# Kernel tuning notes

Measured on AMD Instinct MI355X. Metric: run time of the kernel, lower is better.

## Reference

```python
import jax, jax.numpy as jnp
import numpy as np

B, D_IN, C, P = 8192, 2048, 1000, 256


def setup_inputs() -> dict:
    key = jax.random.key(0)
    ks = jax.random.split(key, 6)
    return {
        "x": jax.random.normal(ks[0], (B, D_IN), dtype=jnp.float32),
        "Wm": jax.random.normal(ks[1], (C, D_IN), dtype=jnp.float32) * (1.0 / np.sqrt(D_IN)),
        "bm": jax.random.normal(ks[2], (C,), dtype=jnp.float32) * 0.01,
        "u": jax.random.normal(ks[3], (P, C), dtype=jnp.float32),
        "v": jax.random.normal(ks[4], (P, C), dtype=jnp.float32),
        "w": jax.random.normal(ks[5], (P, 1), dtype=jnp.float32),
    }


def reference(x, Wm, bm, u, v, w):
    # Backbone: Linear(D_IN -> C) producing per-instance logits (B, C)
    preds = jnp.einsum("bd,cd->bc", x, Wm) + bm
    # Gated attention, fully batched (replaces per-instance Python loop):
    # tanh(u @ pred) * sigmoid(v @ pred)  -> (B, P)
    gated = jnp.tanh(jnp.einsum("bc,pc->bp", preds, u)) * jax.nn.sigmoid(
        jnp.einsum("bc,pc->bp", preds, v)
    )
    scores = (gated @ w).ravel()          # (B,)
    attention = jax.nn.softmax(scores)    # softmax over instances
    total_pred = jnp.sum(preds * attention[:, None])
    return preds, total_pred
```

## Files before the change

kernel.cpp:

```cpp
#include <hip/hip_runtime.h>
#include <hip/hip_fp16.h>

typedef _Float16 half8 __attribute__((ext_vector_type(8)));
typedef float f32x4 __attribute__((ext_vector_type(4)));

#define B_   8192
#define DIN  2048
#define C_   1000
#define CP   1024
#define NP2  512

static const size_t OFF_XH  = 0;
static const size_t OFF_WH  = OFF_XH  + (size_t)B_ * DIN * 2;
static const size_t OFF_UVH = OFF_WH  + (size_t)CP * DIN * 2;
static const size_t OFF_PH  = OFF_UVH + (size_t)NP2 * CP * 2;
static const size_t OFF_SC  = OFF_PH  + (size_t)B_ * CP * 2;
static const size_t OFF_RS  = OFF_SC  + (size_t)B_ * 4;
static const size_t WS_NEED = OFF_RS  + (size_t)B_ * 4;

#define FENCE asm volatile("" ::: "memory")
#define BARRIER do { FENCE; __builtin_amdgcn_s_barrier(); FENCE; } while (0)

__device__ __forceinline__ void gload16(const void* g, void* l) {
  __builtin_amdgcn_global_load_lds(
      (const __attribute__((address_space(1))) void*)g,
      (__attribute__((address_space(3))) void*)l, 16, 0, 0);
}

__global__ __launch_bounds__(256) void prep_kernel(
    const float* __restrict__ x, const float* __restrict__ Wm,
    const float* __restrict__ u, const float* __restrict__ v,
    _Float16* __restrict__ xh, _Float16* __restrict__ wh,
    _Float16* __restrict__ uvh, float* __restrict__ scores,
    float* __restrict__ rowsum)
{
  const long NX  = (long)B_ * DIN / 8;
  const long NW  = (long)CP * DIN / 8;
  const long NUV = (long)NP2 * CP / 8;
  const long NZ  = 2 * (long)B_ / 8;
  const long T   = NX + NW + NUV + NZ;
  for (long idx = (long)blockIdx.x * blockDim.x + threadIdx.x; idx < T;
       idx += (long)gridDim.x * blockDim.x) {
    if (idx < NX) {
      long e = idx * 8;
      float4 p0 = *(const float4*)(x + e);
      float4 p1 = *(const float4*)(x + e + 4);
      half8 h;
      h[0] = (_Float16)p0.x; h[1] = (_Float16)p0.y; h[2] = (_Float16)p0.z; h[3] = (_Float16)p0.w;
      h[4] = (_Float16)p1.x; h[5] = (_Float16)p1.y; h[6] = (_Float16)p1.z; h[7] = (_Float16)p1.w;
      *(half8*)(xh + e) = h;
    } else if (idx < NX + NW) {
      long e = (idx - NX) * 8;
      int row = (int)(e >> 11);
      half8 h;
      if (row < C_) {
        float4 p0 = *(const float4*)(Wm + e);
        float4 p1 = *(const float4*)(Wm + e + 4);
        h[0] = (_Float16)p0.x; h[1] = (_Float16)p0.y; h[2] = (_Float16)p0.z; h[3] = (_Float16)p0.w;
        h[4] = (_Float16)p1.x; h[5] = (_Float16)p1.y; h[6] = (_Float16)p1.z; h[7] = (_Float16)p1.w;
      } else {
        h = (half8)(_Float16)0.f;
      }
      *(half8*)(wh + e) = h;
    } else if (idx < NX + NW + NUV) {
      long e = (idx - NX - NW) * 8;
      int j = (int)(e >> 10);
      int k = (int)(e & 1023);
      const float* src = (j & 1) ? v : u;
      int p = j >> 1;
      half8 h;
      #pragma unroll
      for (int t = 0; t < 8; ++t) {
        int kk = k + t;
        h[t] = (kk < C_) ? (_Float16)src[(size_t)p * C_ + kk] : (_Float16)0.f;
      }
      *(half8*)(uvh + e) = h;
    } else {
      long e = (idx - NX - NW - NUV) * 8;
      float4 z = {0.f, 0.f, 0.f, 0.f};
      if (e < B_) {
        *(float4*)(scores + e) = z; *(float4*)(scores + e + 4) = z;
      } else {
        long r = e - B_;
        *(float4*)(rowsum + r) = z; *(float4*)(rowsum + r + 4) = z;
      }
    }
  }
}

__global__ __launch_bounds__(512) void gemm1_kernel(
    const _Float16* __restrict__ xh, const _Float16* __restrict__ wh,
    const float* __restrict__ bmv, float* __restrict__ preds,
    _Float16* __restrict__ predsh, float* __restrict__ rowsum)
{
  __shared__ _Float16 lds[3 * 24576];
  const int tid  = threadIdx.x;
  const int lane = tid & 63;
  const int w    = tid >> 6;
  const int wm   = w >> 1;
  const int wn   = w & 1;
  const int bm0  = blockIdx.x * 256;
  const int bn0  = blockIdx.y * 128;

  f32x4 acc[4][4] = {};

  const _Float16* srcA[4];
  const _Float16* srcB[2];
  #pragma unroll
  for (int k = 0; k < 4; ++k) {
    int slot = k * 512 + tid;
    int row  = slot >> 3;
    int cb   = (slot & 7) << 4;
    int scb  = cb ^ ((row & 7) << 4);
    srcA[k] = xh + (size_t)(bm0 + row) * DIN + (scb >> 1);
  }
  #pragma unroll
  for (int k = 0; k < 2; ++k) {
    int slot = k * 512 + tid;
    int row  = slot >> 3;
    int cb   = (slot & 7) << 4;
    int scb  = cb ^ ((row & 7) << 4);
    srcB[k] = wh + (size_t)(bn0 + row) * DIN + (scb >> 1);
  }

  int aoff[4][2], boff[4][2];
  #pragma unroll
  for (int m = 0; m < 4; ++m) {
    #pragma unroll
    for (int ks = 0; ks < 2; ++ks) {
      int ra = wm * 64 + m * 16 + (lane & 15);
      int kb = ks * 64 + (lane >> 4) * 16;
      aoff[m][ks] = ra * 128 + (kb ^ ((ra & 7) << 4));
    }
  }
  #pragma unroll
  for (int n = 0; n < 4; ++n) {
    #pragma unroll
    for (int ks = 0; ks < 2; ++ks) {
      int rb = wn * 64 + n * 16 + (lane & 15);
      int kb = ks * 64 + (lane >> 4) * 16;
      boff[n][ks] = 32768 + rb * 128 + (kb ^ ((rb & 7) << 4));
    }
  }

  half8 aLa[2][2], aLb[2][2], aHf[2][2], bLf[2][2], bHf[2][2];

  auto stA = [&](int cs, int k) {
    gload16(srcA[k], (char*)lds + cs * 49152 + k * 8192 + w * 1024);
  };
  auto stB = [&](int cs, int k) {
    gload16(srcB[k], (char*)lds + cs * 49152 + 32768 + k * 8192 + w * 1024);
  };
  auto advance = [&]() {
    #pragma unroll
    for (int k = 0; k < 4; ++k) srcA[k] += 64;
    srcB[0] += 64; srcB[1] += 64;
  };
  auto rdAH = [&](const char* b) {
    #pragma unroll
    for (int m = 0; m < 2; ++m)
      #pragma unroll
      for (int ks = 0; ks < 2; ++ks)
        aHf[m][ks] = *(const half8*)(b + aoff[m + 2][ks]);
  };
  auto rdBH = [&](const char* b) {
    #pragma unroll
    for (int n = 0; n < 2; ++n)
      #pragma unroll
      for (int ks = 0; ks < 2; ++ks)
        bHf[n][ks] = *(const half8*)(b + boff[n + 2][ks]);
  };
  auto rdAL = [&](const char* b, half8 (&d)[2][2]) {
    #pragma unroll
    for (int m = 0; m < 2; ++m)
      #pragma unroll
      for (int ks = 0; ks < 2; ++ks)
        d[m][ks] = *(const half8*)(b + aoff[m][ks]);
  };
  auto rdBL = [&](const char* b) {
    #pragma unroll
    for (int n = 0; n < 2; ++n)
      #pragma unroll
      for (int ks = 0; ks < 2; ++ks)
        bLf[n][ks] = *(const half8*)(b + boff[n][ks]);
  };
  auto mfLL = [&](half8 (&aL)[2][2]) {
    #pragma unroll
    for (int m = 0; m < 2; ++m)
      #pragma unroll
      for (int n = 0; n < 2; ++n)
        #pragma unroll
        for (int ks = 0; ks < 2; ++ks)
          acc[m][n] = __builtin_amdgcn_mfma_f32_16x16x32_f16(aL[m][ks], bLf[n][ks], acc[m][n], 0, 0, 0);
  };
  auto mfHL = [&]() {
    #pragma unroll
    for (int m = 0; m < 2; ++m)
      #pragma unroll
      for (int n = 0; n < 2; ++n)
        #pragma unroll
        for (int ks = 0; ks < 2; ++ks)
          acc[m + 2][n] = __builtin_amdgcn_mfma_f32_16x16x32_f16(aHf[m][ks], bLf[n][ks], acc[m + 2][n], 0, 0, 0);
  };
  auto mfLH = [&](half8 (&aL)[2][2]) {
    #pragma unroll
    for (int m = 0; m < 2; ++m)
      #pragma unroll
      for (int n = 0; n < 2; ++n)
        #pragma unroll
        for (int ks = 0; ks < 2; ++ks)
          acc[m][n + 2] = __builtin_amdgcn_mfma_f32_16x16x32_f16(aL[m][ks], bHf[n][ks], acc[m][n + 2], 0, 0, 0);
  };
  auto mfHH = [&]() {
    #pragma unroll
    for (int m = 0; m < 2; ++m)
      #pragma unroll
      for (int n = 0; n < 2; ++n)
        #pragma unroll
        for (int ks = 0; ks < 2; ++ks)
          acc[m + 2][n + 2] = __builtin_amdgcn_mfma_f32_16x16x32_f16(aHf[m][ks], bHf[n][ks], acc[m + 2][n + 2], 0, 0, 0);
  };

  #pragma unroll
  for (int k = 0; k < 4; ++k) stA(0, k);
  stB(0, 0); stB(0, 1);
  advance();
  #pragma unroll
  for (int k = 0; k < 4; ++k) stA(1, k);
  stB(1, 0); stB(1, 1);
  advance();
  asm volatile("s_waitcnt vmcnt(6)" ::: "memory");
  BARRIER;
  rdAL((const char*)lds, aLa);
  rdBL((const char*)lds);

  int c0 = 0;
  #pragma unroll 1
  for (int t = 0; t < 30; t += 2) {
    const int c1 = (c0 == 2) ? 0 : c0 + 1;
    const int c2 = (c1 == 2) ? 0 : c1 + 1;
    const char* bt  = (const char*)lds + c0 * 49152;
    const char* bn1 = (const char*)lds + c1 * 49152;
    const char* bn2 = (const char*)lds + c2 * 49152;

    rdAH(bt);  stA(c2, 0); stA(c2, 1);
    BARRIER;
    __builtin_amdgcn_s_setprio(1); mfLL(aLa); __builtin_amdgcn_s_setprio(0);

    rdBH(bt);  stA(c2, 2); stA(c2, 3);
    asm volatile("s_waitcnt vmcnt(4)" ::: "memory");
    BARRIER;
    __builtin_amdgcn_s_setprio(1); mfHL(); __builtin_amdgcn_s_setprio(0);

    rdAL(bn1, aLb);  stB(c2, 0);
    BARRIER;
    __builtin_amdgcn_s_setprio(1); mfLH(aLa); __builtin_amdgcn_s_setprio(0);

    rdBL(bn1);  stB(c2, 1); advance();
    BARRIER;
    __builtin_amdgcn_s_setprio(1); mfHH(); __builtin_amdgcn_s_setprio(0);

    rdAH(bn1);  stA(c0, 0); stA(c0, 1);
    BARRIER;
    __builtin_amdgcn_s_setprio(1); mfLL(aLb); __builtin_amdgcn_s_setprio(0);

    rdBH(bn1);  stA(c0, 2); stA(c0, 3);
    asm volatile("s_waitcnt vmcnt(4)" ::: "memory");
    BARRIER;
    __builtin_amdgcn_s_setprio(1); mfHL(); __builtin_amdgcn_s_setprio(0);

    rdAL(bn2, aLa);  stB(c0, 0);
    BARRIER;
    __builtin_amdgcn_s_setprio(1); mfLH(aLb); __builtin_amdgcn_s_setprio(0);

    rdBL(bn2);  stB(c0, 1); advance();
    BARRIER;
    __builtin_amdgcn_s_setprio(1); mfHH(); __builtin_amdgcn_s_setprio(0);

    c0 = c2;
  }

  {
    const char* bt  = (const char*)lds;
    const char* bn1 = (const char*)lds + 49152;
    rdAH(bt);
    BARRIER;
    __builtin_amdgcn_s_setprio(1); mfLL(aLa); __builtin_amdgcn_s_setprio(0);
    rdBH(bt);
    asm volatile("s_waitcnt vmcnt(0)" ::: "memory");
    BARRIER;
    __builtin_amdgcn_s_setprio(1); mfHL(); __builtin_amdgcn_s_setprio(0);
    rdAL(bn1, aLb);
    BARRIER;
    __builtin_amdgcn_s_setprio(1); mfLH(aLa); __builtin_amdgcn_s_setprio(0);
    rdBL(bn1);
    BARRIER;
    __builtin_amdgcn_s_setprio(1); mfHH(); __builtin_amdgcn_s_setprio(0);
    rdAH(bn1); rdBH(bn1);
    mfLL(aLb); mfHL(); mfLH(aLb); mfHH();
  }

  float rp[4][4] = {};
  #pragma unroll
  for (int m = 0; m < 4; ++m) {
    #pragma unroll
    for (int n = 0; n < 4; ++n) {
      f32x4 d = acc[m][n];
      int gc = bn0 + wn * 64 + n * 16 + (lane & 15);
      float bias = (gc < C_) ? bmv[gc] : 0.f;
      #pragma unroll
      for (int j = 0; j < 4; ++j) {
        int gr = bm0 + wm * 64 + m * 16 + (lane >> 4) * 4 + j;
        float val = d[j] + bias;
        predsh[(size_t)gr * CP + gc] = (_Float16)val;
        if (gc < C_) preds[(size_t)gr * C_ + gc] = val;
        rp[m][j] += val;
      }
    }
  }
  #pragma unroll
  for (int m = 0; m < 4; ++m) {
    #pragma unroll
    for (int j = 0; j < 4; ++j) {
      float s = rp[m][j];
      s += __shfl_xor(s, 1); s += __shfl_xor(s, 2);
      s += __shfl_xor(s, 4); s += __shfl_xor(s, 8);
      if ((lane & 15) == 0) {
        int gr = bm0 + wm * 64 + m * 16 + (lane >> 4) * 4 + j;
        atomicAdd(&rowsum[gr], s);
      }
    }
  }
}

__global__ __launch_bounds__(256) void gemm2_kernel(
    const _Float16* __restrict__ predsh, const _Float16* __restrict__ uvh,
    const float* __restrict__ wv, float* __restrict__ scores)
{
  __shared__ _Float16 sA[2][64 * 64];
  __shared__ _Float16 sB[2][128 * 64];
  const int tid  = threadIdx.x;
  const int lane = tid & 63;
  const int w    = tid >> 6;
  const int wm   = w >> 1, wn = w & 1;
  const int bm0  = blockIdx.x * 64;
  const int bn0  = blockIdx.y * 128;

  f32x4 acc[2][4] = {};

  const _Float16* srcA[2]; const _Float16* srcB[4];
  #pragma unroll
  for (int i = 0; i < 2; ++i) {
    int slot = i * 256 + tid;
    int row  = slot >> 3;
    int cb   = (slot & 7) << 4;
    int scb  = cb ^ ((row & 7) << 4);
    srcA[i] = predsh + (size_t)(bm0 + row) * CP + (scb >> 1);
  }
  #pragma unroll
  for (int i = 0; i < 4; ++i) {
    int slot = i * 256 + tid;
    int row  = slot >> 3;
    int cb   = (slot & 7) << 4;
    int scb  = cb ^ ((row & 7) << 4);
    srcB[i] = uvh + (size_t)(bn0 + row) * CP + (scb >> 1);
  }
  int aoff[2][2], boff[4][2];
  #pragma unroll
  for (int ks = 0; ks < 2; ++ks) {
    int kb = ks * 64 + (lane >> 4) * 16;
    #pragma unroll
    for (int mi = 0; mi < 2; ++mi) {
      int ra = wm * 32 + mi * 16 + (lane & 15);
      aoff[mi][ks] = ra * 128 + (kb ^ ((ra & 7) << 4));
    }
    #pragma unroll
    for (int ni = 0; ni < 4; ++ni) {
      int rb = wn * 64 + ni * 16 + (lane & 15);
      boff[ni][ks] = rb * 128 + (kb ^ ((rb & 7) << 4));
    }
  }

  auto stage = [&](int c) {
    #pragma unroll
    for (int i = 0; i < 2; ++i) {
      gload16(srcA[i], &sA[c][(i * 4 + w) * 512]);
      srcA[i] += 64;
    }
    #pragma unroll
    for (int i = 0; i < 4; ++i) {
      gload16(srcB[i], &sB[c][(i * 4 + w) * 512]);
      srcB[i] += 64;
    }
  };

  auto compute = [&](int c) {
    const char* bA = (const char*)&sA[c][0];
    const char* bB = (const char*)&sB[c][0];
    #pragma unroll
    for (int ks = 0; ks < 2; ++ks) {
      half8 a[2], b[4];
      #pragma unroll
      for (int mi = 0; mi < 2; ++mi) a[mi] = *(const half8*)(bA + aoff[mi][ks]);
      #pragma unroll
      for (int ni = 0; ni < 4; ++ni) b[ni] = *(const half8*)(bB + boff[ni][ks]);
      #pragma unroll
      for (int mi = 0; mi < 2; ++mi)
        #pragma unroll
        for (int ni = 0; ni < 4; ++ni)
          acc[mi][ni] = __builtin_amdgcn_mfma_f32_16x16x32_f16(a[mi], b[ni], acc[mi][ni], 0, 0, 0);
    }
  };

  const int NT = CP / 64;
  stage(0);
  #pragma unroll 1
  for (int kt = 0; kt < NT; kt += 2) {
    stage(1);
    asm volatile("s_waitcnt vmcnt(6)" ::: "memory");
    BARRIER;
    compute(0);
    BARRIER;
    if (kt + 2 < NT) {
      stage(0);
      asm volatile("s_waitcnt vmcnt(6)" ::: "memory");
    } else {
      asm volatile("s_waitcnt vmcnt(0)" ::: "memory");
    }
    BARRIER;
    compute(1);
    BARRIER;
  }

  float sp[2][4] = {};
  #pragma unroll
  for (int mi = 0; mi < 2; ++mi) {
    #pragma unroll
    for (int ni = 0; ni < 4; ++ni) {
      f32x4 d = acc[mi][ni];
      int gc = bn0 + wn * 64 + ni * 16 + (lane & 15);
      float wq = wv[gc >> 1];
      bool even = ((gc & 1) == 0);
      #pragma unroll
      for (int j = 0; j < 4; ++j) {
        float t  = d[j];
        float pr = __shfl_xor(t, 1);
        float th = 2.f / (1.f + __expf(-2.f * t)) - 1.f;
        float sg = 1.f / (1.f + __expf(-pr));
        sp[mi][j] += even ? (th * sg * wq) : 0.f;
      }
    }
  }
  #pragma unroll
  for (int mi = 0; mi < 2; ++mi) {
    #pragma unroll
    for (int j = 0; j < 4; ++j) {
      float s = sp[mi][j];
      s += __shfl_xor(s, 1); s += __shfl_xor(s, 2);
      s += __shfl_xor(s, 4); s += __shfl_xor(s, 8);
      if ((lane & 15) == 0) {
        int gr = bm0 + wm * 32 + mi * 16 + (lane >> 4) * 4 + j;
        atomicAdd(&scores[gr], s);
      }
    }
  }
}

__global__ __launch_bounds__(1024) void final_kernel(
    const float* __restrict__ scores, const float* __restrict__ rowsum,
    float* __restrict__ out)
{
  __shared__ float red[16], red2[16];
  const int t = threadIdx.x;
  const int lane = t & 63, wid = t >> 6;
  float s[8];
  float m = -3.4e38f;
  #pragma unroll
  for (int i = 0; i < 8; ++i) { s[i] = scores[t + i * 1024]; m = fmaxf(m, s[i]); }
  #pragma unroll
  for (int off = 1; off < 64; off <<= 1) m = fmaxf(m, __shfl_xor(m, off));
  if (lane == 0) red[wid] = m;
  __syncthreads();
  #pragma unroll
  for (int i = 0; i < 16; ++i) m = fmaxf(m, red[i]);
  __syncthreads();

  float se = 0.f, sr = 0.f;
  #pragma unroll
  for (int i = 0; i < 8; ++i) {
    float e = __expf(s[i] - m);
    se += e;
    sr += e * rowsum[t + i * 1024];
  }
  #pragma unroll
  for (int off = 1; off < 64; off <<= 1) { se += __shfl_xor(se, off); sr += __shfl_xor(sr, off); }
  if (lane == 0) { red[wid] = se; red2[wid] = sr; }
  __syncthreads();
  if (t == 0) {
    float tse = 0.f, tsr = 0.f;
    for (int i = 0; i < 16; ++i) { tse += red[i]; tsr += red2[i]; }
    out[0] = tsr / tse;
  }
}

extern "C" void kernel_launch(void* const* d_in, const int* in_sizes, int n_in,
                              void* d_out, int out_size, void* d_ws, size_t ws_size,
                              hipStream_t stream)
{
  const float* x   = (const float*)d_in[0];
  const float* Wm  = (const float*)d_in[1];
  const float* bmv = (const float*)d_in[2];
  const float* u   = (const float*)d_in[3];
  const float* v   = (const float*)d_in[4];
  const float* wv  = (const float*)d_in[5];
  float* out = (float*)d_out;

  if (ws_size < WS_NEED) return;

  char* ws = (char*)d_ws;
  _Float16* xh     = (_Float16*)(ws + OFF_XH);
  _Float16* wh     = (_Float16*)(ws + OFF_WH);
  _Float16* uvh    = (_Float16*)(ws + OFF_UVH);
  _Float16* predsh = (_Float16*)(ws + OFF_PH);
  float*    scores = (float*)(ws + OFF_SC);
  float*    rowsum = (float*)(ws + OFF_RS);

  prep_kernel<<<2048, 256, 0, stream>>>(x, Wm, u, v, xh, wh, uvh, scores, rowsum);
  gemm1_kernel<<<dim3(32, 8), 512, 0, stream>>>(xh, wh, bmv, out, predsh, rowsum);
  gemm2_kernel<<<dim3(128, 4), 256, 0, stream>>>(predsh, uvh, wv, scores);
  final_kernel<<<1, 1024, 0, stream>>>(scores, rowsum, out + (size_t)B_ * C_);
}
```

Baseline: 90.41 us.

## Fuse fp32-to-fp16 conversion of x into GEMM1 load pipeline

Drops the separate pass that converts x to fp16 in the prep kernel. GEMM1 now loads fp32 x tiles into registers, converts them and writes the swizzled fp16 tiles to LDS, and the software pipeline is restructured around these register loads and their waitcnts. This removes a 64MB read plus 32MB write and re-read of the xh buffer. In exchange, GEMM1 reads x as fp32, which is twice the global bytes that were previously read from the fp16 copy. It also adds VALU conversion work and LDS stores that run inside the main loop alongside the MFMAs.

```diff
diff --git a/kernel.cpp b/kernel.cpp
--- a/kernel.cpp
+++ b/kernel.cpp
@@ -10,8 +10,7 @@
 #define CP   1024
 #define NP2  512
 
-static const size_t OFF_XH  = 0;
-static const size_t OFF_WH  = OFF_XH  + (size_t)B_ * DIN * 2;
+static const size_t OFF_WH  = 0;
 static const size_t OFF_UVH = OFF_WH  + (size_t)CP * DIN * 2;
 static const size_t OFF_PH  = OFF_UVH + (size_t)NP2 * CP * 2;
 static const size_t OFF_SC  = OFF_PH  + (size_t)B_ * CP * 2;
@@ -20,6 +19,8 @@
 
 #define FENCE asm volatile("" ::: "memory")
 #define BARRIER do { FENCE; __builtin_amdgcn_s_barrier(); FENCE; } while (0)
+#define VMCNT(n) asm volatile("s_waitcnt vmcnt(" #n ")" ::: "memory")
+#define LGKM0    asm volatile("s_waitcnt lgkmcnt(0)" ::: "memory")
 
 __device__ __forceinline__ void gload16(const void* g, void* l) {
   __builtin_amdgcn_global_load_lds(
@@ -28,29 +29,19 @@
 }
 
 __global__ __launch_bounds__(256) void prep_kernel(
-    const float* __restrict__ x, const float* __restrict__ Wm,
+    const float* __restrict__ Wm,
     const float* __restrict__ u, const float* __restrict__ v,
-    _Float16* __restrict__ xh, _Float16* __restrict__ wh,
-    _Float16* __restrict__ uvh, float* __restrict__ scores,
-    float* __restrict__ rowsum)
+    _Float16* __restrict__ wh, _Float16* __restrict__ uvh,
+    float* __restrict__ scores, float* __restrict__ rowsum)
 {
-  const long NX  = (long)B_ * DIN / 8;
   const long NW  = (long)CP * DIN / 8;
   const long NUV = (long)NP2 * CP / 8;
   const long NZ  = 2 * (long)B_ / 8;
-  const long T   = NX + NW + NUV + NZ;
+  const long T   = NW + NUV + NZ;
   for (long idx = (long)blockIdx.x * blockDim.x + threadIdx.x; idx < T;
        idx += (long)gridDim.x * blockDim.x) {
-    if (idx < NX) {
+    if (idx < NW) {
       long e = idx * 8;
-      float4 p0 = *(const float4*)(x + e);
-      float4 p1 = *(const float4*)(x + e + 4);
-      half8 h;
-      h[0] = (_Float16)p0.x; h[1] = (_Float16)p0.y; h[2] = (_Float16)p0.z; h[3] = (_Float16)p0.w;
-      h[4] = (_Float16)p1.x; h[5] = (_Float16)p1.y; h[6] = (_Float16)p1.z; h[7] = (_Float16)p1.w;
-      *(half8*)(xh + e) = h;
-    } else if (idx < NX + NW) {
-      long e = (idx - NX) * 8;
       int row = (int)(e >> 11);
       half8 h;
       if (row < C_) {
@@ -62,8 +53,8 @@
         h = (half8)(_Float16)0.f;
       }
       *(half8*)(wh + e) = h;
-    } else if (idx < NX + NW + NUV) {
-      long e = (idx - NX - NW) * 8;
+    } else if (idx < NW + NUV) {
+      long e = (idx - NW) * 8;
       int j = (int)(e >> 10);
       int k = (int)(e & 1023);
       const float* src = (j & 1) ? v : u;
@@ -76,7 +67,7 @@
       }
       *(half8*)(uvh + e) = h;
     } else {
-      long e = (idx - NX - NW - NUV) * 8;
+      long e = (idx - NW - NUV) * 8;
       float4 z = {0.f, 0.f, 0.f, 0.f};
       if (e < B_) {
         *(float4*)(scores + e) = z; *(float4*)(scores + e + 4) = z;
@@ -89,11 +80,12 @@
 }
 
 __global__ __launch_bounds__(512) void gemm1_kernel(
-    const _Float16* __restrict__ xh, const _Float16* __restrict__ wh,
+    const float* __restrict__ x, const _Float16* __restrict__ wh,
     const float* __restrict__ bmv, float* __restrict__ preds,
     _Float16* __restrict__ predsh, float* __restrict__ rowsum)
 {
-  __shared__ _Float16 lds[3 * 24576];
+  __shared__ _Float16 lds[3 * 16384 + 3 * 8192];
+  char* const LB = (char*)lds;
   const int tid  = threadIdx.x;
   const int lane = tid & 63;
   const int w    = tid >> 6;
@@ -104,16 +96,17 @@
 
   f32x4 acc[4][4] = {};
 
-  const _Float16* srcA[4];
+  const float* srcAx[4];
+  int dstAoff[4];
+  #pragma unroll
+  for (int j = 0; j < 4; ++j) {
+    int slot = j * 512 + tid;
+    int row  = slot >> 3;
+    int col8 = slot & 7;
+    srcAx[j]   = x + (size_t)(bm0 + row) * DIN + col8 * 8;
+    dstAoff[j] = row * 128 + ((col8 << 4) ^ ((row & 7) << 4));
+  }
   const _Float16* srcB[2];
-  #pragma unroll
-  for (int k = 0; k < 4; ++k) {
-    int slot = k * 512 + tid;
-    int row  = slot >> 3;
-    int cb   = (slot & 7) << 4;
-    int scb  = cb ^ ((row & 7) << 4);
-    srcA[k] = xh + (size_t)(bm0 + row) * DIN + (scb >> 1);
-  }
   #pragma unroll
   for (int k = 0; k < 2; ++k) {
     int slot = k * 512 + tid;
@@ -139,21 +132,38 @@
     for (int ks = 0; ks < 2; ++ks) {
       int rb = wn * 64 + n * 16 + (lane & 15);
       int kb = ks * 64 + (lane >> 4) * 16;
-      boff[n][ks] = 32768 + rb * 128 + (kb ^ ((rb & 7) << 4));
+      boff[n][ks] = rb * 128 + (kb ^ ((rb & 7) << 4));
     }
   }
 
   half8 aLa[2][2], aLb[2][2], aHf[2][2], bLf[2][2], bHf[2][2];
-
-  auto stA = [&](int cs, int k) {
-    gload16(srcA[k], (char*)lds + cs * 49152 + k * 8192 + w * 1024);
-  };
-  auto stB = [&](int cs, int k) {
-    gload16(srcB[k], (char*)lds + cs * 49152 + 32768 + k * 8192 + w * 1024);
-  };
-  auto advance = [&]() {
-    #pragma unroll
-    for (int k = 0; k < 4; ++k) srcA[k] += 64;
+  float4 af[4][2];
+
+  auto issueA01 = [&]() {
+    af[0][0] = *(const float4*)srcAx[0]; af[0][1] = *(const float4*)(srcAx[0] + 4);
+    af[1][0] = *(const float4*)srcAx[1]; af[1][1] = *(const float4*)(srcAx[1] + 4);
+  };
+  auto issueA23 = [&]() {
+    af[2][0] = *(const float4*)srcAx[2]; af[2][1] = *(const float4*)(srcAx[2] + 4);
+    af[3][0] = *(const float4*)srcAx[3]; af[3][1] = *(const float4*)(srcAx[3] + 4);
+    #pragma unroll
+    for (int j = 0; j < 4; ++j) srcAx[j] += 64;
+  };
+  auto cvtWriteA = [&](int cbuf) {
+    char* base = LB + cbuf * 32768;
+    #pragma unroll
+    for (int j = 0; j < 4; ++j) {
+      half8 h;
+      h[0] = (_Float16)af[j][0].x; h[1] = (_Float16)af[j][0].y;
+      h[2] = (_Float16)af[j][0].z; h[3] = (_Float16)af[j][0].w;
+      h[4] = (_Float16)af[j][1].x; h[5] = (_Float16)af[j][1].y;
+      h[6] = (_Float16)af[j][1].z; h[7] = (_Float16)af[j][1].w;
+      *(half8*)(base + dstAoff[j]) = h;
+    }
+  };
+  auto stB = [&](int cbuf) {
+    gload16(srcB[0], LB + 98304 + cbuf * 16384 + w * 1024);
+    gload16(srcB[1], LB + 98304 + cbuf * 16384 + 8192 + w * 1024);
     srcB[0] += 64; srcB[1] += 64;
   };
   auto rdAH = [&](const char* b) {
@@ -221,82 +231,101 @@
           acc[m + 2][n + 2] = __builtin_amdgcn_mfma_f32_16x16x32_f16(aHf[m][ks], bHf[n][ks], acc[m + 2][n + 2], 0, 0, 0);
   };
 
-  #pragma unroll
-  for (int k = 0; k < 4; ++k) stA(0, k);
-  stB(0, 0); stB(0, 1);
-  advance();
-  #pragma unroll
-  for (int k = 0; k < 4; ++k) stA(1, k);
-  stB(1, 0); stB(1, 1);
-  advance();
-  asm volatile("s_waitcnt vmcnt(6)" ::: "memory");
+  #define PRIO1 __builtin_amdgcn_s_setprio(1)
+  #define PRIO0 __builtin_amdgcn_s_setprio(0)
+
+  issueA01(); issueA23();
+  stB(0);
+  VMCNT(2);
+  cvtWriteA(0);
+  issueA01(); issueA23();
+  stB(1);
+  VMCNT(10);
+  LGKM0;
   BARRIER;
-  rdAL((const char*)lds, aLa);
-  rdBL((const char*)lds);
+  rdAL(LB, aLa);
+  rdBL(LB + 98304);
 
   int c0 = 0;
   #pragma unroll 1
   for (int t = 0; t < 30; t += 2) {
     const int c1 = (c0 == 2) ? 0 : c0 + 1;
     const int c2 = (c1 == 2) ? 0 : c1 + 1;
-    const char* bt  = (const char*)lds + c0 * 49152;
-    const char* bn1 = (const char*)lds + c1 * 49152;
-    const char* bn2 = (const char*)lds + c2 * 49152;
-
-    rdAH(bt);  stA(c2, 0); stA(c2, 1);
-    BARRIER;
-    __builtin_amdgcn_s_setprio(1); mfLL(aLa); __builtin_amdgcn_s_setprio(0);
-
-    rdBH(bt);  stA(c2, 2); stA(c2, 3);
-    asm volatile("s_waitcnt vmcnt(4)" ::: "memory");
-    BARRIER;
-    __builtin_amdgcn_s_setprio(1); mfHL(); __builtin_amdgcn_s_setprio(0);
-
-    rdAL(bn1, aLb);  stB(c2, 0);
-    BARRIER;
-    __builtin_amdgcn_s_setprio(1); mfLH(aLa); __builtin_amdgcn_s_setprio(0);
-
-    rdBL(bn1);  stB(c2, 1); advance();
-    BARRIER;
-    __builtin_amdgcn_s_setprio(1); mfHH(); __builtin_amdgcn_s_setprio(0);
-
-    rdAH(bn1);  stA(c0, 0); stA(c0, 1);
-    BARRIER;
-    __builtin_amdgcn_s_setprio(1); mfLL(aLb); __builtin_amdgcn_s_setprio(0);
-
-    rdBH(bn1);  stA(c0, 2); stA(c0, 3);
-    asm volatile("s_waitcnt vmcnt(4)" ::: "memory");
-    BARRIER;
-    __builtin_amdgcn_s_setprio(1); mfHL(); __builtin_amdgcn_s_setprio(0);
-
-    rdAL(bn2, aLa);  stB(c0, 0);
-    BARRIER;
-    __builtin_amdgcn_s_setprio(1); mfLH(aLb); __builtin_amdgcn_s_setprio(0);
-
-    rdBL(bn2);  stB(c0, 1); advance();
-    BARRIER;
-    __builtin_amdgcn_s_setprio(1); mfHH(); __builtin_amdgcn_s_setprio(0);
+    const char* pA0 = LB + c0 * 32768;
+    const char* pA1 = LB + c1 * 32768;
+    const char* pA2 = LB + c2 * 32768;
+    const char* pB0 = LB + 98304 + c0 * 16384;
+    const char* pB1 = LB + 98304 + c1 * 16384;
+    const char* pB2 = LB + 98304 + c2 * 16384;
+
+    VMCNT(2);
+    cvtWriteA(c1);
+    rdAH(pA0);
+    issueA01();
+    LGKM0; BARRIER;
+    PRIO1; mfLL(aLa); PRIO0;
+
+    rdBH(pB0);
+    issueA23();
+    BARRIER;
+    PRIO1; mfHL(); PRIO0;
+
+    rdAL(pA1, aLb);
+    stB(c2);
+    BARRIER;
+    PRIO1; mfLH(aLa); PRIO0;
+
+    VMCNT(10);
+    BARRIER;
+    rdBL(pB1);
+    PRIO1; mfHH(); PRIO0;
+
+    VMCNT(2);
+    cvtWriteA(c2);
+    rdAH(pA1);
+    issueA01();
+    LGKM0; BARRIER;
+    PRIO1; mfLL(aLb); PRIO0;
+
+    rdBH(pB1);
+    issueA23();
+    BARRIER;
+    PRIO1; mfHL(); PRIO0;
+
+    rdAL(pA2, aLa);
+    stB(c0);
+    BARRIER;
+    PRIO1; mfLH(aLb); PRIO0;
+
+    VMCNT(10);
+    BARRIER;
+    rdBL(pB2);
+    PRIO1; mfHH(); PRIO0;
 
     c0 = c2;
   }
 
   {
-    const char* bt  = (const char*)lds;
-    const char* bn1 = (const char*)lds + 49152;
-    rdAH(bt);
-    BARRIER;
-    __builtin_amdgcn_s_setprio(1); mfLL(aLa); __builtin_amdgcn_s_setprio(0);
-    rdBH(bt);
-    asm volatile("s_waitcnt vmcnt(0)" ::: "memory");
-    BARRIER;
-    __builtin_amdgcn_s_setprio(1); mfHL(); __builtin_amdgcn_s_setprio(0);
-    rdAL(bn1, aLb);
-    BARRIER;
-    __builtin_amdgcn_s_setprio(1); mfLH(aLa); __builtin_amdgcn_s_setprio(0);
-    rdBL(bn1);
-    BARRIER;
-    __builtin_amdgcn_s_setprio(1); mfHH(); __builtin_amdgcn_s_setprio(0);
-    rdAH(bn1); rdBH(bn1);
+    const char* pA0 = LB;
+    const char* pA1 = LB + 32768;
+    const char* pB0 = LB + 98304;
+    const char* pB1 = LB + 98304 + 16384;
+    VMCNT(2);
+    cvtWriteA(1);
+    rdAH(pA0);
+    LGKM0; BARRIER;
+    PRIO1; mfLL(aLa); PRIO0;
+    rdBH(pB0);
+    BARRIER;
+    PRIO1; mfHL(); PRIO0;
+    rdAL(pA1, aLb);
+    BARRIER;
+    PRIO1; mfLH(aLa); PRIO0;
+    VMCNT(0);
+    BARRIER;
+    rdBL(pB1);
+    PRIO1; mfHH(); PRIO0;
+    rdAH(pA1); rdBH(pB1);
     mfLL(aLb); mfHL(); mfLH(aLb); mfHH();
   }
 
@@ -331,6 +360,8 @@
       }
     }
   }
+  #undef PRIO1
+  #undef PRIO0
 }
 
 __global__ __launch_bounds__(256) void gemm2_kernel(
@@ -518,15 +549,14 @@
   if (ws_size < WS_NEED) return;
 
   char* ws = (char*)d_ws;
-  _Float16* xh     = (_Float16*)(ws + OFF_XH);
   _Float16* wh     = (_Float16*)(ws + OFF_WH);
   _Float16* uvh    = (_Float16*)(ws + OFF_UVH);
   _Float16* predsh = (_Float16*)(ws + OFF_PH);
   float*    scores = (float*)(ws + OFF_SC);
   float*    rowsum = (float*)(ws + OFF_RS);
 
-  prep_kernel<<<2048, 256, 0, stream>>>(x, Wm, u, v, xh, wh, uvh, scores, rowsum);
-  gemm1_kernel<<<dim3(32, 8), 512, 0, stream>>>(xh, wh, bmv, out, predsh, rowsum);
+  prep_kernel<<<1288, 256, 0, stream>>>(Wm, u, v, wh, uvh, scores, rowsum);
+  gemm1_kernel<<<dim3(32, 8), 512, 0, stream>>>(x, wh, bmv, out, predsh, rowsum);
   gemm2_kernel<<<dim3(128, 4), 256, 0, stream>>>(predsh, uvh, wv, scores);
   final_kernel<<<1, 1024, 0, stream>>>(scores, rowsum, out + (size_t)B_ * C_);
 }
```

After: 91.46 us. Within noise of the previous version (+1.2%).

## Enlarge per-wave tiles and triple-buffer both GEMM kernels with finer-grained pipeline

Applied to the files above, without the earlier changes.

gemm1 drops from 512 to 256 threads per block while keeping the 256x128 block tile, so each wave now computes a 128x64 tile with 32 accumulators. The main loop is also rewritten to one K-step per iteration with interleaved quarter-tile MFMA groups. gemm2 moves from a double-buffered 64x128 tile to a triple-buffered 128x128 tile using the same four-phase staggered LDS read / global-to-LDS load schedule, which halves its grid. The aim is to raise MFMA work per LDS read and improve overlap of loads with compute, at the cost of higher register pressure (launch_bounds 256,1) and fewer waves per CU to hide latency.

```diff
diff --git a/kernel.cpp b/kernel.cpp
--- a/kernel.cpp
+++ b/kernel.cpp
@@ -20,6 +20,9 @@
 
 #define FENCE asm volatile("" ::: "memory")
 #define BARRIER do { FENCE; __builtin_amdgcn_s_barrier(); FENCE; } while (0)
+#define VMCNT(n) asm volatile("s_waitcnt vmcnt(" #n ")" ::: "memory")
+#define PRIO1 __builtin_amdgcn_s_setprio(1)
+#define PRIO0 __builtin_amdgcn_s_setprio(0)
 
 __device__ __forceinline__ void gload16(const void* g, void* l) {
   __builtin_amdgcn_global_load_lds(
@@ -88,12 +91,13 @@
   }
 }
 
-__global__ __launch_bounds__(512) void gemm1_kernel(
+__global__ __launch_bounds__(256, 1) void gemm1_kernel(
     const _Float16* __restrict__ xh, const _Float16* __restrict__ wh,
     const float* __restrict__ bmv, float* __restrict__ preds,
     _Float16* __restrict__ predsh, float* __restrict__ rowsum)
 {
-  __shared__ _Float16 lds[3 * 24576];
+  __shared__ _Float16 lds[(3 * 32768 + 3 * 16384) / 2];
+  char* const LB = (char*)lds;
   const int tid  = threadIdx.x;
   const int lane = tid & 63;
   const int w    = tid >> 6;
@@ -102,207 +106,176 @@
   const int bm0  = blockIdx.x * 256;
   const int bn0  = blockIdx.y * 128;
 
-  f32x4 acc[4][4] = {};
-
-  const _Float16* srcA[4];
-  const _Float16* srcB[2];
-  #pragma unroll
-  for (int k = 0; k < 4; ++k) {
-    int slot = k * 512 + tid;
-    int row  = slot >> 3;
-    int cb   = (slot & 7) << 4;
-    int scb  = cb ^ ((row & 7) << 4);
-    srcA[k] = xh + (size_t)(bm0 + row) * DIN + (scb >> 1);
-  }
-  #pragma unroll
-  for (int k = 0; k < 2; ++k) {
-    int slot = k * 512 + tid;
-    int row  = slot >> 3;
-    int cb   = (slot & 7) << 4;
-    int scb  = cb ^ ((row & 7) << 4);
-    srcB[k] = wh + (size_t)(bn0 + row) * DIN + (scb >> 1);
-  }
-
-  int aoff[4][2], boff[4][2];
-  #pragma unroll
-  for (int m = 0; m < 4; ++m) {
+  f32x4 acc[8][4] = {};
+
+  const int trow = tid >> 3;
+  const int swzc = (((tid & 7) << 4) ^ ((trow & 7) << 4)) >> 1;
+  const _Float16* pA = xh + (size_t)(bm0 + trow) * DIN + swzc;
+  const _Float16* pB = wh + (size_t)(bn0 + trow) * DIN + swzc;
+
+  int aoff[8][2], boff[4][2];
+  #pragma unroll
+  for (int m = 0; m < 8; ++m)
     #pragma unroll
     for (int ks = 0; ks < 2; ++ks) {
-      int ra = wm * 64 + m * 16 + (lane & 15);
+      int ra = wm * 128 + m * 16 + (lane & 15);
       int kb = ks * 64 + (lane >> 4) * 16;
       aoff[m][ks] = ra * 128 + (kb ^ ((ra & 7) << 4));
     }
-  }
-  #pragma unroll
-  for (int n = 0; n < 4; ++n) {
+  #pragma unroll
+  for (int n = 0; n < 4; ++n)
     #pragma unroll
     for (int ks = 0; ks < 2; ++ks) {
       int rb = wn * 64 + n * 16 + (lane & 15);
       int kb = ks * 64 + (lane >> 4) * 16;
-      boff[n][ks] = 32768 + rb * 128 + (kb ^ ((rb & 7) << 4));
-    }
-  }
-
-  half8 aLa[2][2], aLb[2][2], aHf[2][2], bLf[2][2], bHf[2][2];
-
-  auto stA = [&](int cs, int k) {
-    gload16(srcA[k], (char*)lds + cs * 49152 + k * 8192 + w * 1024);
-  };
-  auto stB = [&](int cs, int k) {
-    gload16(srcB[k], (char*)lds + cs * 49152 + 32768 + k * 8192 + w * 1024);
-  };
-  auto advance = [&]() {
-    #pragma unroll
-    for (int k = 0; k < 4; ++k) srcA[k] += 64;
-    srcB[0] += 64; srcB[1] += 64;
-  };
-  auto rdAH = [&](const char* b) {
-    #pragma unroll
-    for (int m = 0; m < 2; ++m)
-      #pragma unroll
-      for (int ks = 0; ks < 2; ++ks)
-        aHf[m][ks] = *(const half8*)(b + aoff[m + 2][ks]);
-  };
-  auto rdBH = [&](const char* b) {
+      boff[n][ks] = rb * 128 + (kb ^ ((rb & 7) << 4));
+    }
+
+  half8 A[8][2], Bf[4][2];
+
+  auto stA = [&](int c, int k) {
+    gload16(pA + (size_t)k * 32 * DIN, LB + c * 32768 + k * 4096 + w * 1024);
+  };
+  auto stB = [&](int c, int k) {
+    gload16(pB + (size_t)k * 32 * DIN, LB + 98304 + c * 16384 + k * 4096 + w * 1024);
+  };
+  auto advance = [&]() { pA += 64; pB += 64; };
+
+  auto rdAL = [&](int c) {
+    const char* b = LB + c * 32768;
+    #pragma unroll
+    for (int m = 0; m < 4; ++m)
+      #pragma unroll
+      for (int ks = 0; ks < 2; ++ks)
+        A[m][ks] = *(const half8*)(b + aoff[m][ks]);
+  };
+  auto rdAH = [&](int c) {
+    const char* b = LB + c * 32768;
+    #pragma unroll
+    for (int m = 4; m < 8; ++m)
+      #pragma unroll
+      for (int ks = 0; ks < 2; ++ks)
+        A[m][ks] = *(const half8*)(b + aoff[m][ks]);
+  };
+  auto rdBL = [&](int c) {
+    const char* b = LB + 98304 + c * 16384;
     #pragma unroll
     for (int n = 0; n < 2; ++n)
       #pragma unroll
       for (int ks = 0; ks < 2; ++ks)
-        bHf[n][ks] = *(const half8*)(b + boff[n + 2][ks]);
-  };
-  auto rdAL = [&](const char* b, half8 (&d)[2][2]) {
-    #pragma unroll
-    for (int m = 0; m < 2; ++m)
-      #pragma unroll
-      for (int ks = 0; ks < 2; ++ks)
-        d[m][ks] = *(const half8*)(b + aoff[m][ks]);
-  };
-  auto rdBL = [&](const char* b) {
-    #pragma unroll
-    for (int n = 0; n < 2; ++n)
-      #pragma unroll
-      for (int ks = 0; ks < 2; ++ks)
-        bLf[n][ks] = *(const half8*)(b + boff[n][ks]);
-  };
-  auto mfLL = [&](half8 (&aL)[2][2]) {
-    #pragma unroll
-    for (int m = 0; m < 2; ++m)
+        Bf[n][ks] = *(const half8*)(b + boff[n][ks]);
+  };
+  auto rdBH = [&](int c) {
+    const char* b = LB + 98304 + c * 16384;
+    #pragma unroll
+    for (int n = 2; n < 4; ++n)
+      #pragma unroll
+      for (int ks = 0; ks < 2; ++ks)
+        Bf[n][ks] = *(const half8*)(b + boff[n][ks]);
+  };
+  auto mfALBL = [&]() {
+    #pragma unroll
+    for (int m = 0; m < 4; ++m)
       #pragma unroll
       for (int n = 0; n < 2; ++n)
         #pragma unroll
         for (int ks = 0; ks < 2; ++ks)
-          acc[m][n] = __builtin_amdgcn_mfma_f32_16x16x32_f16(aL[m][ks], bLf[n][ks], acc[m][n], 0, 0, 0);
-  };
-  auto mfHL = [&]() {
-    #pragma unroll
-    for (int m = 0; m < 2; ++m)
+          acc[m][n] = __builtin_amdgcn_mfma_f32_16x16x32_f16(A[m][ks], Bf[n][ks], acc[m][n], 0, 0, 0);
+  };
+  auto mfAHBL = [&]() {
+    #pragma unroll
+    for (int m = 4; m < 8; ++m)
       #pragma unroll
       for (int n = 0; n < 2; ++n)
         #pragma unroll
         for (int ks = 0; ks < 2; ++ks)
-          acc[m + 2][n] = __builtin_amdgcn_mfma_f32_16x16x32_f16(aHf[m][ks], bLf[n][ks], acc[m + 2][n], 0, 0, 0);
-  };
-  auto mfLH = [&](half8 (&aL)[2][2]) {
-    #pragma unroll
-    for (int m = 0; m < 2; ++m)
-      #pragma unroll
-      for (int n = 0; n < 2; ++n)
+          acc[m][n] = __builtin_amdgcn_mfma_f32_16x16x32_f16(A[m][ks], Bf[n][ks], acc[m][n], 0, 0, 0);
+  };
+  auto mfALBH = [&]() {
+    #pragma unroll
+    for (int m = 0; m < 4; ++m)
+      #pragma unroll
+      for (int n = 2; n < 4; ++n)
         #pragma unroll
         for (int ks = 0; ks < 2; ++ks)
-          acc[m][n + 2] = __builtin_amdgcn_mfma_f32_16x16x32_f16(aL[m][ks], bHf[n][ks], acc[m][n + 2], 0, 0, 0);
-  };
-  auto mfHH = [&]() {
-    #pragma unroll
-    for (int m = 0; m < 2; ++m)
-      #pragma unroll
-      for (int n = 0; n < 2; ++n)
+          acc[m][n] = __builtin_amdgcn_mfma_f32_16x16x32_f16(A[m][ks], Bf[n][ks], acc[m][n], 0, 0, 0);
+  };
+  auto mfAHBH = [&]() {
+    #pragma unroll
+    for (int m = 4; m < 8; ++m)
+      #pragma unroll
+      for (int n = 2; n < 4; ++n)
         #pragma unroll
         for (int ks = 0; ks < 2; ++ks)
-          acc[m + 2][n + 2] = __builtin_amdgcn_mfma_f32_16x16x32_f16(aHf[m][ks], bHf[n][ks], acc[m + 2][n + 2], 0, 0, 0);
-  };
-
-  #pragma unroll
-  for (int k = 0; k < 4; ++k) stA(0, k);
-  stB(0, 0); stB(0, 1);
+          acc[m][n] = __builtin_amdgcn_mfma_f32_16x16x32_f16(A[m][ks], Bf[n][ks], acc[m][n], 0, 0, 0);
+  };
+
+  #pragma unroll
+  for (int k = 0; k < 8; ++k) stA(0, k);
+  #pragma unroll
+  for (int k = 0; k < 4; ++k) stB(0, k);
   advance();
   #pragma unroll
-  for (int k = 0; k < 4; ++k) stA(1, k);
-  stB(1, 0); stB(1, 1);
+  for (int k = 0; k < 8; ++k) stA(1, k);
+  #pragma unroll
+  for (int k = 0; k < 4; ++k) stB(1, k);
   advance();
-  asm volatile("s_waitcnt vmcnt(6)" ::: "memory");
+  VMCNT(12);
   BARRIER;
-  rdAL((const char*)lds, aLa);
-  rdBL((const char*)lds);
+  rdAL(0); rdBL(0);
 
   int c0 = 0;
   #pragma unroll 1
-  for (int t = 0; t < 30; t += 2) {
+  for (int t = 0; t < 30; ++t) {
     const int c1 = (c0 == 2) ? 0 : c0 + 1;
     const int c2 = (c1 == 2) ? 0 : c1 + 1;
-    const char* bt  = (const char*)lds + c0 * 49152;
-    const char* bn1 = (const char*)lds + c1 * 49152;
-    const char* bn2 = (const char*)lds + c2 * 49152;
-
-    rdAH(bt);  stA(c2, 0); stA(c2, 1);
-    BARRIER;
-    __builtin_amdgcn_s_setprio(1); mfLL(aLa); __builtin_amdgcn_s_setprio(0);
-
-    rdBH(bt);  stA(c2, 2); stA(c2, 3);
-    asm volatile("s_waitcnt vmcnt(4)" ::: "memory");
-    BARRIER;
-    __builtin_amdgcn_s_setprio(1); mfHL(); __builtin_amdgcn_s_setprio(0);
-
-    rdAL(bn1, aLb);  stB(c2, 0);
-    BARRIER;
-    __builtin_amdgcn_s_setprio(1); mfLH(aLa); __builtin_amdgcn_s_setprio(0);
-
-    rdBL(bn1);  stB(c2, 1); advance();
-    BARRIER;
-    __builtin_amdgcn_s_setprio(1); mfHH(); __builtin_amdgcn_s_setprio(0);
-
-    rdAH(bn1);  stA(c0, 0); stA(c0, 1);
-    BARRIER;
-    __builtin_amdgcn_s_setprio(1); mfLL(aLb); __builtin_amdgcn_s_setprio(0);
-
-    rdBH(bn1);  stA(c0, 2); stA(c0, 3);
-    asm volatile("s_waitcnt vmcnt(4)" ::: "memory");
-    BARRIER;
-    __builtin_amdgcn_s_setprio(1); mfHL(); __builtin_amdgcn_s_setprio(0);
-
-    rdAL(bn2, aLa);  stB(c0, 0);
-    BARRIER;
-    __builtin_amdgcn_s_setprio(1); mfLH(aLb); __builtin_amdgcn_s_setprio(0);
-
-    rdBL(bn2);  stB(c0, 1); advance();
-    BARRIER;
-    __builtin_amdgcn_s_setprio(1); mfHH(); __builtin_amdgcn_s_setprio(0);
-
-    c0 = c2;
+
+    rdAH(c0);
+    stA(c2, 0); stA(c2, 1); stA(c2, 2);
+    BARRIER;
+    PRIO1; mfALBL(); PRIO0;
+
+    rdBH(c0);
+    stA(c2, 3); stA(c2, 4); stA(c2, 5);
+    VMCNT(6);
+    BARRIER;
+    PRIO1; mfAHBL(); PRIO0;
+
+    rdBL(c1);
+    stA(c2, 6); stA(c2, 7); stB(c2, 0);
+    BARRIER;
+    PRIO1; mfALBH(); PRIO0;
+
+    rdAL(c1);
+    stB(c2, 1); stB(c2, 2); stB(c2, 3);
+    advance();
+    BARRIER;
+    PRIO1; mfAHBH(); PRIO0;
+
+    c0 = c1;
   }
 
   {
-    const char* bt  = (const char*)lds;
-    const char* bn1 = (const char*)lds + 49152;
-    rdAH(bt);
-    BARRIER;
-    __builtin_amdgcn_s_setprio(1); mfLL(aLa); __builtin_amdgcn_s_setprio(0);
-    rdBH(bt);
-    asm volatile("s_waitcnt vmcnt(0)" ::: "memory");
-    BARRIER;
-    __builtin_amdgcn_s_setprio(1); mfHL(); __builtin_amdgcn_s_setprio(0);
-    rdAL(bn1, aLb);
-    BARRIER;
-    __builtin_amdgcn_s_setprio(1); mfLH(aLa); __builtin_amdgcn_s_setprio(0);
-    rdBL(bn1);
-    BARRIER;
-    __builtin_amdgcn_s_setprio(1); mfHH(); __builtin_amdgcn_s_setprio(0);
-    rdAH(bn1); rdBH(bn1);
-    mfLL(aLb); mfHL(); mfLH(aLb); mfHH();
-  }
-
-  float rp[4][4] = {};
-  #pragma unroll
-  for (int m = 0; m < 4; ++m) {
+    rdAH(0);
+    BARRIER;
+    PRIO1; mfALBL(); PRIO0;
+    rdBH(0);
+    VMCNT(0);
+    BARRIER;
+    PRIO1; mfAHBL(); PRIO0;
+    rdBL(1);
+    BARRIER;
+    PRIO1; mfALBH(); PRIO0;
+    rdAL(1);
+    BARRIER;
+    PRIO1; mfAHBH(); PRIO0;
+    rdAH(1); rdBH(1);
+    mfALBL(); mfAHBL(); mfALBH(); mfAHBH();
+  }
+
+  float rp[8][4] = {};
+  #pragma unroll
+  for (int m = 0; m < 8; ++m) {
     #pragma unroll
     for (int n = 0; n < 4; ++n) {
       f32x4 d = acc[m][n];
@@ -310,7 +283,7 @@
       float bias = (gc < C_) ? bmv[gc] : 0.f;
       #pragma unroll
       for (int j = 0; j < 4; ++j) {
-        int gr = bm0 + wm * 64 + m * 16 + (lane >> 4) * 4 + j;
+        int gr = bm0 + wm * 128 + m * 16 + (lane >> 4) * 4 + j;
         float val = d[j] + bias;
         predsh[(size_t)gr * CP + gc] = (_Float16)val;
         if (gc < C_) preds[(size_t)gr * C_ + gc] = val;
@@ -319,122 +292,173 @@
     }
   }
   #pragma unroll
-  for (int m = 0; m < 4; ++m) {
+  for (int m = 0; m < 8; ++m) {
     #pragma unroll
     for (int j = 0; j < 4; ++j) {
       float s = rp[m][j];
       s += __shfl_xor(s, 1); s += __shfl_xor(s, 2);
       s += __shfl_xor(s, 4); s += __shfl_xor(s, 8);
       if ((lane & 15) == 0) {
-        int gr = bm0 + wm * 64 + m * 16 + (lane >> 4) * 4 + j;
+        int gr = bm0 + wm * 128 + m * 16 + (lane >> 4) * 4 + j;
         atomicAdd(&rowsum[gr], s);
       }
     }
   }
 }
 
-__global__ __launch_bounds__(256) void gemm2_kernel(
+__global__ __launch_bounds__(256, 1) void gemm2_kernel(
     const _Float16* __restrict__ predsh, const _Float16* __restrict__ uvh,
     const float* __restrict__ wv, float* __restrict__ scores)
 {
-  __shared__ _Float16 sA[2][64 * 64];
-  __shared__ _Float16 sB[2][128 * 64];
+  __shared__ _Float16 lds2[(3 * 16384 + 3 * 16384) / 2];
+  char* const LB = (char*)lds2;
   const int tid  = threadIdx.x;
   const int lane = tid & 63;
   const int w    = tid >> 6;
   const int wm   = w >> 1, wn = w & 1;
-  const int bm0  = blockIdx.x * 64;
+  const int bm0  = blockIdx.x * 128;
   const int bn0  = blockIdx.y * 128;
 
-  f32x4 acc[2][4] = {};
-
-  const _Float16* srcA[2]; const _Float16* srcB[4];
-  #pragma unroll
-  for (int i = 0; i < 2; ++i) {
-    int slot = i * 256 + tid;
-    int row  = slot >> 3;
-    int cb   = (slot & 7) << 4;
-    int scb  = cb ^ ((row & 7) << 4);
-    srcA[i] = predsh + (size_t)(bm0 + row) * CP + (scb >> 1);
-  }
-  #pragma unroll
-  for (int i = 0; i < 4; ++i) {
-    int slot = i * 256 + tid;
-    int row  = slot >> 3;
-    int cb   = (slot & 7) << 4;
-    int scb  = cb ^ ((row & 7) << 4);
-    srcB[i] = uvh + (size_t)(bn0 + row) * CP + (scb >> 1);
-  }
-  int aoff[2][2], boff[4][2];
-  #pragma unroll
-  for (int ks = 0; ks < 2; ++ks) {
-    int kb = ks * 64 + (lane >> 4) * 16;
-    #pragma unroll
-    for (int mi = 0; mi < 2; ++mi) {
-      int ra = wm * 32 + mi * 16 + (lane & 15);
-      aoff[mi][ks] = ra * 128 + (kb ^ ((ra & 7) << 4));
-    }
-    #pragma unroll
-    for (int ni = 0; ni < 4; ++ni) {
-      int rb = wn * 64 + ni * 16 + (lane & 15);
-      boff[ni][ks] = rb * 128 + (kb ^ ((rb & 7) << 4));
-    }
-  }
-
-  auto stage = [&](int c) {
-    #pragma unroll
-    for (int i = 0; i < 2; ++i) {
-      gload16(srcA[i], &sA[c][(i * 4 + w) * 512]);
-      srcA[i] += 64;
-    }
-    #pragma unroll
-    for (int i = 0; i < 4; ++i) {
-      gload16(srcB[i], &sB[c][(i * 4 + w) * 512]);
-      srcB[i] += 64;
-    }
-  };
-
-  auto compute = [&](int c) {
-    const char* bA = (const char*)&sA[c][0];
-    const char* bB = (const char*)&sB[c][0];
+  f32x4 acc[4][4] = {};
+
+  const int trow = tid >> 3;
+  const int swzc = (((tid & 7) << 4) ^ ((trow & 7) << 4)) >> 1;
+  const _Float16* pA = predsh + (size_t)(bm0 + trow) * CP + swzc;
+  const _Float16* pB = uvh    + (size_t)(bn0 + trow) * CP + swzc;
+
+  int aoff[4][2], boff[4][2];
+  #pragma unroll
+  for (int m = 0; m < 4; ++m)
     #pragma unroll
     for (int ks = 0; ks < 2; ++ks) {
-      half8 a[2], b[4];
-      #pragma unroll
-      for (int mi = 0; mi < 2; ++mi) a[mi] = *(const half8*)(bA + aoff[mi][ks]);
-      #pragma unroll
-      for (int ni = 0; ni < 4; ++ni) b[ni] = *(const half8*)(bB + boff[ni][ks]);
-      #pragma unroll
-      for (int mi = 0; mi < 2; ++mi)
+      int ra = wm * 64 + m * 16 + (lane & 15);
+      int kb = ks * 64 + (lane >> 4) * 16;
+      aoff[m][ks] = ra * 128 + (kb ^ ((ra & 7) << 4));
+    }
+  #pragma unroll
+  for (int n = 0; n < 4; ++n)
+    #pragma unroll
+    for (int ks = 0; ks < 2; ++ks) {
+      int rb = wn * 64 + n * 16 + (lane & 15);
+      int kb = ks * 64 + (lane >> 4) * 16;
+      boff[n][ks] = rb * 128 + (kb ^ ((rb & 7) << 4));
+    }
+
+  half8 A[4][2], Bf[4][2];
+
+  auto stA = [&](int c, int k) {
+    gload16(pA + (size_t)k * 32 * CP, LB + c * 16384 + k * 4096 + w * 1024);
+  };
+  auto stB = [&](int c, int k) {
+    gload16(pB + (size_t)k * 32 * CP, LB + 49152 + c * 16384 + k * 4096 + w * 1024);
+  };
+  auto advance = [&]() { pA += 64; pB += 64; };
+
+  auto rdAL = [&](int c) {
+    const char* b = LB + c * 16384;
+    #pragma unroll
+    for (int m = 0; m < 2; ++m)
+      #pragma unroll
+      for (int ks = 0; ks < 2; ++ks)
+        A[m][ks] = *(const half8*)(b + aoff[m][ks]);
+  };
+  auto rdAH = [&](int c) {
+    const char* b = LB + c * 16384;
+    #pragma unroll
+    for (int m = 2; m < 4; ++m)
+      #pragma unroll
+      for (int ks = 0; ks < 2; ++ks)
+        A[m][ks] = *(const half8*)(b + aoff[m][ks]);
+  };
+  auto rdBL = [&](int c) {
+    const char* b = LB + 49152 + c * 16384;
+    #pragma unroll
+    for (int n = 0; n < 2; ++n)
+      #pragma unroll
+      for (int ks = 0; ks < 2; ++ks)
+        Bf[n][ks] = *(const half8*)(b + boff[n][ks]);
+  };
+  auto rdBH = [&](int c) {
+    const char* b = LB + 49152 + c * 16384;
+    #pragma unroll
+    for (int n = 2; n < 4; ++n)
+      #pragma unroll
+      for (int ks = 0; ks < 2; ++ks)
+        Bf[n][ks] = *(const half8*)(b + boff[n][ks]);
+  };
+  auto mf = [&](int mlo, int nlo) {
+    #pragma unroll
+    for (int m = 0; m < 2; ++m)
+      #pragma unroll
+      for (int n = 0; n < 2; ++n)
         #pragma unroll
-        for (int ni = 0; ni < 4; ++ni)
-          acc[mi][ni] = __builtin_amdgcn_mfma_f32_16x16x32_f16(a[mi], b[ni], acc[mi][ni], 0, 0, 0);
-    }
-  };
-
-  const int NT = CP / 64;
-  stage(0);
+        for (int ks = 0; ks < 2; ++ks)
+          acc[mlo + m][nlo + n] = __builtin_amdgcn_mfma_f32_16x16x32_f16(
+              A[mlo + m][ks], Bf[nlo + n][ks], acc[mlo + m][nlo + n], 0, 0, 0);
+  };
+
+  #pragma unroll
+  for (int k = 0; k < 4; ++k) stA(0, k);
+  #pragma unroll
+  for (int k = 0; k < 4; ++k) stB(0, k);
+  advance();
+  #pragma unroll
+  for (int k = 0; k < 4; ++k) stA(1, k);
+  #pragma unroll
+  for (int k = 0; k < 4; ++k) stB(1, k);
+  advance();
+  VMCNT(8);
+  BARRIER;
+  rdAL(0); rdBL(0);
+
+  int c0 = 0;
   #pragma unroll 1
-  for (int kt = 0; kt < NT; kt += 2) {
-    stage(1);
-    asm volatile("s_waitcnt vmcnt(6)" ::: "memory");
-    BARRIER;
-    compute(0);
-    BARRIER;
-    if (kt + 2 < NT) {
-      stage(0);
-      asm volatile("s_waitcnt vmcnt(6)" ::: "memory");
-    } else {
-      asm volatile("s_waitcnt vmcnt(0)" ::: "memory");
-    }
-    BARRIER;
-    compute(1);
-    BARRIER;
-  }
-
-  float sp[2][4] = {};
-  #pragma unroll
-  for (int mi = 0; mi < 2; ++mi) {
+  for (int t = 0; t < 14; ++t) {
+    const int c1 = (c0 == 2) ? 0 : c0 + 1;
+    const int c2 = (c1 == 2) ? 0 : c1 + 1;
+
+    rdAH(c0);  stA(c2, 0); stA(c2, 1);
+    BARRIER;
+    PRIO1; mf(0, 0); PRIO0;
+
+    rdBH(c0);  stA(c2, 2); stA(c2, 3);
+    VMCNT(4);
+    BARRIER;
+    PRIO1; mf(2, 0); PRIO0;
+
+    rdBL(c1);  stB(c2, 0); stB(c2, 1);
+    BARRIER;
+    PRIO1; mf(0, 2); PRIO0;
+
+    rdAL(c1);  stB(c2, 2); stB(c2, 3);
+    advance();
+    BARRIER;
+    PRIO1; mf(2, 2); PRIO0;
+
+    c0 = c1;
+  }
+  {
+    const int c0t = 2, c1t = 0;
+    rdAH(c0t);
+    BARRIER;
+    PRIO1; mf(0, 0); PRIO0;
+    rdBH(c0t);
+    VMCNT(0);
+    BARRIER;
+    PRIO1; mf(2, 0); PRIO0;
+    rdBL(c1t);
+    BARRIER;
+    PRIO1; mf(0, 2); PRIO0;
+    rdAL(c1t);
+    BARRIER;
+    PRIO1; mf(2, 2); PRIO0;
+    rdAH(c1t); rdBH(c1t);
+    mf(0, 0); mf(2, 0); mf(0, 2); mf(2, 2);
+  }
+
+  float sp[4][4] = {};
+  #pragma unroll
+  for (int mi = 0; mi < 4; ++mi) {
     #pragma unroll
     for (int ni = 0; ni < 4; ++ni) {
       f32x4 d = acc[mi][ni];
@@ -452,14 +476,14 @@
     }
   }
   #pragma unroll
-  for (int mi = 0; mi < 2; ++mi) {
+  for (int mi = 0; mi < 4; ++mi) {
     #pragma unroll
     for (int j = 0; j < 4; ++j) {
       float s = sp[mi][j];
       s += __shfl_xor(s, 1); s += __shfl_xor(s, 2);
       s += __shfl_xor(s, 4); s += __shfl_xor(s, 8);
       if ((lane & 15) == 0) {
-        int gr = bm0 + wm * 32 + mi * 16 + (lane >> 4) * 4 + j;
+        int gr = bm0 + wm * 64 + mi * 16 + (lane >> 4) * 4 + j;
         atomicAdd(&scores[gr], s);
       }
     }
@@ -526,7 +550,7 @@
   float*    rowsum = (float*)(ws + OFF_RS);
 
   prep_kernel<<<2048, 256, 0, stream>>>(x, Wm, u, v, xh, wh, uvh, scores, rowsum);
-  gemm1_kernel<<<dim3(32, 8), 512, 0, stream>>>(xh, wh, bmv, out, predsh, rowsum);
-  gemm2_kernel<<<dim3(128, 4), 256, 0, stream>>>(predsh, uvh, wv, scores);
+  gemm1_kernel<<<dim3(32, 8), 256, 0, stream>>>(xh, wh, bmv, out, predsh, rowsum);
+  gemm2_kernel<<<dim3(64, 4), 256, 0, stream>>>(predsh, uvh, wv, scores);
   final_kernel<<<1, 1024, 0, stream>>>(scores, rowsum, out + (size_t)B_ * C_);
 }
```

Result: slower. 103.1 us (+14.0%).
